# Optimization experiments

Measured on AMD Instinct MI355X. Metric: run time of the kernel, lower is better.

Reference implementation:

```python
import jax, jax.numpy as jnp
import numpy as np

B, T, N, D, H = 2, 12, 1024, 128, 8
HD = D // H  # head_dim = 16


def setup_inputs() -> dict:
    key = jax.random.key(0)
    ks = jax.random.split(key, 11)
    std = 0.02
    return {
        "query": jax.random.normal(ks[0], (B, T, N, D), dtype=jnp.float32),
        "key": jax.random.normal(ks[1], (B, T, N, D), dtype=jnp.float32),
        "value": jax.random.normal(ks[2], (B, T, N, D), dtype=jnp.float32),
        "Wq": jax.random.normal(ks[3], (D, D), dtype=jnp.float32) * std,
        "bq": jnp.zeros((D,), dtype=jnp.float32),
        "Wk": jax.random.normal(ks[4], (D, D), dtype=jnp.float32) * std,
        "bk": jnp.zeros((D,), dtype=jnp.float32),
        "Wv": jax.random.normal(ks[5], (D, D), dtype=jnp.float32) * std,
        "bv": jnp.zeros((D,), dtype=jnp.float32),
        "Wo": jax.random.normal(ks[6], (D, D), dtype=jnp.float32) * std,
        "bo": jnp.zeros((D,), dtype=jnp.float32),
    }


def reference(query, key, value, Wq, bq, Wk, bk, Wv, bv, Wo, bo):
    # Linear projections (torch nn.Linear: x @ W.T + b)
    q = query @ Wq.T + bq   # (B,T,N,D)
    k = key @ Wk.T + bk
    v = value @ Wv.T + bv
    # split heads: last dim D -> (H, HD)
    q = q.reshape(B, T, N, H, HD)
    k = k.reshape(B, T, N, H, HD)
    v = v.reshape(B, T, N, H, HD)
    scale = 1.0 / jnp.sqrt(jnp.float32(HD))
    # attention across node dim (N); scores (B,H,T,N,N) ~ 805 MB
    scores = jnp.einsum('btnhd,btmhd->bhtnm', q, k) * scale
    attn = jax.nn.softmax(scores, axis=-1)
    out = jnp.einsum('bhtnm,btmhd->btnhd', attn, v)  # (B,T,N,H,HD)
    out = out.reshape(B, T, N, D)
    return out @ Wo.T + bo
```

## Files before the change

### kernel.cpp

```cpp
#include <hip/hip_runtime.h>


#define DEV __device__ __forceinline__

typedef __attribute__((ext_vector_type(4))) float f32x4;
typedef __attribute__((ext_vector_type(8))) short s16x8;
typedef __attribute__((ext_vector_type(4))) short s16x4;
typedef __attribute__((ext_vector_type(2))) unsigned int u32x2;
typedef __attribute__((ext_vector_type(4))) unsigned int u32x4;

DEV unsigned short f2bf(float f) {
    unsigned u = __builtin_bit_cast(unsigned, f);
    u = (u + 0x7fffu + ((u >> 16) & 1u)) >> 16;
    return (unsigned short)u;
}

DEV unsigned pack_bf16(float a, float b) {
#if __has_builtin(__builtin_amdgcn_cvt_pk_bf16_f32)
    typedef __attribute__((ext_vector_type(2))) __bf16 bf16x2;
    bf16x2 t = __builtin_amdgcn_cvt_pk_bf16_f32(a, b);
    return __builtin_bit_cast(unsigned, t);
#else
    unsigned ua = __builtin_bit_cast(unsigned, a) + 0x8000u;
    unsigned ub = __builtin_bit_cast(unsigned, b) + 0x8000u;
    return __builtin_amdgcn_perm(ub, ua, 0x07060302);
#endif
}

DEV f32x4 mfma16(s16x4 a, s16x4 b, f32x4 c) {
#if __has_builtin(__builtin_amdgcn_mfma_f32_16x16x16bf16_1k)
    return __builtin_amdgcn_mfma_f32_16x16x16bf16_1k(a, b, c, 0, 0, 0);
#else
    s16x8 a8 = {a[0], a[1], a[2], a[3], 0, 0, 0, 0};
    s16x8 b8 = {b[0], b[1], b[2], b[3], 0, 0, 0, 0};
    return __builtin_amdgcn_mfma_f32_16x16x32_bf16(a8, b8, c, 0, 0, 0);
#endif
}

DEV f32x4 mfma32(s16x8 a, s16x8 b, f32x4 c) {
    return __builtin_amdgcn_mfma_f32_16x16x32_bf16(a, b, c, 0, 0, 0);
}

__global__ __launch_bounds__(256)
void wconv_kernel(const float* __restrict__ w0, const float* __restrict__ w1,
                  const float* __restrict__ w2, const float* __restrict__ w3,
                  unsigned short* __restrict__ o0, unsigned short* __restrict__ o1,
                  unsigned short* __restrict__ o2, unsigned short* __restrict__ o3)
{
    const int m = blockIdx.x >> 4;
    const float* W = (m == 0) ? w0 : (m == 1) ? w1 : (m == 2) ? w2 : w3;
    unsigned short* o = (m == 0) ? o0 : (m == 1) ? o1 : (m == 2) ? o2 : o3;
    const int idx = (blockIdx.x & 15) * 1024 + threadIdx.x * 4;
    float4 v = *(const float4*)(W + idx);
    ushort4 d;
    d.x = f2bf(v.x); d.y = f2bf(v.y); d.z = f2bf(v.z); d.w = f2bf(v.w);
    *(ushort4*)(o + idx) = d;
}

__global__ __launch_bounds__(256)
void qkv_proj_kernel(const float* __restrict__ xq, const float* __restrict__ xk,
                     const float* __restrict__ xv,
                     const unsigned short* __restrict__ Wqb,
                     const unsigned short* __restrict__ Wkb,
                     const unsigned short* __restrict__ Wvb,
                     const float* __restrict__ bq, const float* __restrict__ bk,
                     const float* __restrict__ bv,
                     unsigned short* __restrict__ oq, unsigned short* __restrict__ ok,
                     unsigned short* __restrict__ ov)
{
    const int z = blockIdx.y;
    const float* X    = (z == 0) ? xq : (z == 1) ? xk : xv;
    const unsigned short* Wb = (z == 0) ? Wqb : (z == 1) ? Wkb : Wvb;
    const float* bias = (z == 0) ? bq : (z == 1) ? bk : bv;
    unsigned short* out = (z == 0) ? oq : (z == 1) ? ok : ov;
    const float scale = (z == 0) ? 0.25f * 1.44269504088896f : 1.0f;

    __shared__ unsigned short Xs[64 * 136];
    __shared__ unsigned short Ws[128 * 136];

    const int t  = threadIdx.x;
    const int m0 = blockIdx.x * 64;

    {
        const float4* Xg = (const float4*)(X + (size_t)m0 * 128);
        #pragma unroll
        for (int p = 0; p < 8; p++) {
            int g = p * 256 + t;
            float4 vv = Xg[g];
            int row = g >> 5, c4 = g & 31;
            ushort4 d;
            d.x = f2bf(vv.x); d.y = f2bf(vv.y); d.z = f2bf(vv.z); d.w = f2bf(vv.w);
            *(ushort4*)&Xs[row * 136 + c4 * 4] = d;
        }
        #pragma unroll
        for (int p = 0; p < 8; p++) {
            int g = p * 256 + t, row = g >> 4, ch = g & 15;
            *(s16x8*)&Ws[row * 136 + ch * 8] =
                *(const s16x8*)(Wb + (size_t)row * 128 + ch * 8);
        }
    }
    __syncthreads();

    const int wave = t >> 6, lane = t & 63, quad = lane >> 4, n16 = lane & 15;
    f32x4 acc[8];
    const f32x4 zero4 = {0.f, 0.f, 0.f, 0.f};
    #pragma unroll
    for (int i = 0; i < 8; i++) acc[i] = zero4;

    #pragma unroll
    for (int ks = 0; ks < 4; ks++) {
        s16x8 a = *(const s16x8*)&Xs[(wave * 16 + n16) * 136 + ks * 32 + quad * 8];
        #pragma unroll
        for (int nt = 0; nt < 8; nt++) {
            s16x8 b = *(const s16x8*)&Ws[(nt * 16 + n16) * 136 + ks * 32 + quad * 8];
            acc[nt] = __builtin_amdgcn_mfma_f32_16x16x32_bf16(a, b, acc[nt], 0, 0, 0);
        }
    }

    const int bt    = m0 >> 10;
    const int nbase = (m0 & 1023) + wave * 16 + quad * 4;
    if (z == 2) {
        #pragma unroll
        for (int nt = 0; nt < 8; nt++) {
            float bb = bias[nt * 16 + n16];
            u32x2 pv = {pack_bf16(acc[nt][0] + bb, acc[nt][1] + bb),
                        pack_bf16(acc[nt][2] + bb, acc[nt][3] + bb)};
            *(u32x2*)&out[((size_t)(bt * 8 + nt) * 16 + n16) * 1024 + nbase] = pv;
        }
    } else {
        __syncthreads();
        const int crow = wave * 16 + quad * 4;
        #pragma unroll
        for (int nt = 0; nt < 8; nt++) {
            float bb = bias[nt * 16 + n16];
            #pragma unroll
            for (int r = 0; r < 4; r++)
                Xs[(crow + r) * 136 + nt * 16 + n16] = f2bf((acc[nt][r] + bb) * scale);
        }
        __syncthreads();
        #pragma unroll
        for (int p = 0; p < 4; p++) {
            int g = p * 256 + t, row = g >> 4, ch = g & 15;
            s16x8 val = *(const s16x8*)&Xs[row * 136 + ch * 8];
            *(s16x8*)&out[((size_t)(bt * 8 + (ch >> 1)) * 1024 + (m0 & 1023) + row) * 16
                          + (ch & 1) * 8] = val;
        }
    }
}

__global__ __launch_bounds__(256)
void attn_kernel(const unsigned short* __restrict__ q,
                 const unsigned short* __restrict__ k,
                 const unsigned short* __restrict__ vt,
                 unsigned short* __restrict__ O)
{
    __shared__ unsigned short Ks[2][256 * 20];
    __shared__ unsigned short VTs[2][16 * 264];

    const int t    = threadIdx.x;
    const int lane = t & 63, quad = lane >> 4, n16 = lane & 15;
    const int wave = t >> 6;
    const int bx = blockIdx.x, h = blockIdx.y, bt = blockIdx.z;
    const size_t headoff = (size_t)(bt * 8 + h) * 16384;
    const int q0 = bx * 64 + wave * 16;

    s16x4 qf = *(const s16x4*)(q + headoff + (size_t)(q0 + n16) * 16 + quad * 4);

    const f32x4 zero4 = {0.f, 0.f, 0.f, 0.f};
    f32x4 oacc = zero4, dacc = zero4;
    const s16x8 ones = {0x3F80, 0x3F80, 0x3F80, 0x3F80,
                        0x3F80, 0x3F80, 0x3F80, 0x3F80};
    const int krd0 = (8 * (n16 >> 2) + (n16 & 3)) * 20 + quad * 4;
    const int vrd  = n16 * 264 + quad * 8;
    const int krow = t >> 2, kseg = (t & 3) * 4;
    const int vrow = t >> 5, vseg = (t & 31) * 8;
    const unsigned short* kg = k  + headoff + (size_t)krow * 16 + kseg;
    const unsigned short* vg = vt + headoff + (size_t)vrow * 1024 + vseg;

    #pragma unroll
    for (int p = 0; p < 4; p++)
        *(s16x4*)&Ks[0][(p * 64 + krow) * 20 + kseg] =
            *(const s16x4*)(kg + (size_t)p * 1024);
    #pragma unroll
    for (int p = 0; p < 2; p++)
        *(s16x8*)&VTs[0][(p * 8 + vrow) * 264 + vseg] =
            *(const s16x8*)(vg + (size_t)p * 8192);

    #pragma unroll
    for (int c = 0; c < 4; c++) {
        __syncthreads();
        s16x4 kst[4];
        s16x8 vst[2];
        if (c < 3) {
            #pragma unroll
            for (int p = 0; p < 4; p++)
                kst[p] = *(const s16x4*)(kg + (size_t)((c + 1) * 256 + p * 64) * 16);
            #pragma unroll
            for (int p = 0; p < 2; p++)
                vst[p] = *(const s16x8*)(vg + (c + 1) * 256 + (size_t)p * 8192);
        }
        const unsigned short* Kc = Ks[c & 1];
        const unsigned short* Vc = VTs[c & 1];
        #pragma unroll
        for (int w = 0; w < 8; w++) {
            s16x4 kf0 = *(const s16x4*)&Kc[w * 640 + krd0];
            s16x4 kf1 = *(const s16x4*)&Kc[w * 640 + krd0 + 80];
            f32x4 s0 = mfma16(kf0, qf, zero4);
            f32x4 s1 = mfma16(kf1, qf, zero4);
            float p0 = __builtin_amdgcn_exp2f(s0[0]);
            float p1 = __builtin_amdgcn_exp2f(s0[1]);
            float p2 = __builtin_amdgcn_exp2f(s0[2]);
            float p3 = __builtin_amdgcn_exp2f(s0[3]);
            float p4 = __builtin_amdgcn_exp2f(s1[0]);
            float p5 = __builtin_amdgcn_exp2f(s1[1]);
            float p6 = __builtin_amdgcn_exp2f(s1[2]);
            float p7 = __builtin_amdgcn_exp2f(s1[3]);
            u32x4 pp = {pack_bf16(p0, p1), pack_bf16(p2, p3),
                        pack_bf16(p4, p5), pack_bf16(p6, p7)};
            s16x8 pf = __builtin_bit_cast(s16x8, pp);
            s16x8 vf = *(const s16x8*)&Vc[w * 32 + vrd];
            oacc = mfma32(pf, vf, oacc);
            dacc = mfma32(pf, ones, dacc);
        }
        if (c < 3) {
            unsigned short* Kn = Ks[(c + 1) & 1];
            unsigned short* Vn = VTs[(c + 1) & 1];
            #pragma unroll
            for (int p = 0; p < 4; p++)
                *(s16x4*)&Kn[(p * 64 + krow) * 20 + kseg] = kst[p];
            #pragma unroll
            for (int p = 0; p < 2; p++)
                *(s16x8*)&Vn[(p * 8 + vrow) * 264 + vseg] = vst[p];
        }
    }

    const int orow = q0 + quad * 4;
    #pragma unroll
    for (int r = 0; r < 4; r++) {
        float rv = oacc[r] * __builtin_amdgcn_rcpf(dacc[r]);
        O[((size_t)bt * 1024 + orow + r) * 128 + h * 16 + n16] = f2bf(rv);
    }
}

__global__ __launch_bounds__(256)
void o_proj_kernel(const unsigned short* __restrict__ X,
                   const unsigned short* __restrict__ Wb,
                   const float* __restrict__ bias, float* __restrict__ out)
{
    __shared__ unsigned short Xs[64 * 136];
    __shared__ unsigned short Ws[128 * 136];

    const int t  = threadIdx.x;
    const int m0 = blockIdx.x * 64;

    {
        #pragma unroll
        for (int p = 0; p < 4; p++) {
            int g = p * 256 + t, row = g >> 4, ch = g & 15;
            *(s16x8*)&Xs[row * 136 + ch * 8] =
                *(const s16x8*)(X + (size_t)(m0 + row) * 128 + ch * 8);
        }
        #pragma unroll
        for (int p = 0; p < 8; p++) {
            int g = p * 256 + t, row = g >> 4, ch = g & 15;
            *(s16x8*)&Ws[row * 136 + ch * 8] =
                *(const s16x8*)(Wb + (size_t)row * 128 + ch * 8);
        }
    }
    __syncthreads();

    const int wave = t >> 6, lane = t & 63, quad = lane >> 4, n16 = lane & 15;
    f32x4 acc[8];
    const f32x4 zero4 = {0.f, 0.f, 0.f, 0.f};
    #pragma unroll
    for (int i = 0; i < 8; i++) acc[i] = zero4;

    #pragma unroll
    for (int ks = 0; ks < 4; ks++) {
        s16x8 a = *(const s16x8*)&Xs[(wave * 16 + n16) * 136 + ks * 32 + quad * 8];
        #pragma unroll
        for (int nt = 0; nt < 8; nt++) {
            s16x8 b = *(const s16x8*)&Ws[(nt * 16 + n16) * 136 + ks * 32 + quad * 8];
            acc[nt] = __builtin_amdgcn_mfma_f32_16x16x32_bf16(a, b, acc[nt], 0, 0, 0);
        }
    }

    const int mrow = m0 + wave * 16 + quad * 4;
    #pragma unroll
    for (int nt = 0; nt < 8; nt++) {
        float bb = bias[nt * 16 + n16];
        #pragma unroll
        for (int r = 0; r < 4; r++)
            out[(size_t)(mrow + r) * 128 + nt * 16 + n16] = acc[nt][r] + bb;
    }
}

extern "C" void kernel_launch(void* const* d_in, const int* in_sizes, int n_in,
                              void* d_out, int out_size, void* d_ws, size_t ws_size,
                              hipStream_t stream)
{
    const float* query = (const float*)d_in[0];
    const float* key_  = (const float*)d_in[1];
    const float* value = (const float*)d_in[2];
    const float* Wq = (const float*)d_in[3];
    const float* bq = (const float*)d_in[4];
    const float* Wk = (const float*)d_in[5];
    const float* bk = (const float*)d_in[6];
    const float* Wv = (const float*)d_in[7];
    const float* bv = (const float*)d_in[8];
    const float* Wo = (const float*)d_in[9];
    const float* bo = (const float*)d_in[10];
    float* out = (float*)d_out;

    char* ws = (char*)d_ws;
    unsigned short* qb  = (unsigned short*)(ws);
    unsigned short* kb  = (unsigned short*)(ws + 6291456);
    unsigned short* vb  = (unsigned short*)(ws + 12582912);
    unsigned short* Ob  = (unsigned short*)(ws + 18874368);
    unsigned short* Wqb = (unsigned short*)(ws + 25165824);
    unsigned short* Wkb = (unsigned short*)(ws + 25198592);
    unsigned short* Wvb = (unsigned short*)(ws + 25231360);
    unsigned short* Wob = (unsigned short*)(ws + 25264128);

    wconv_kernel<<<dim3(64, 1, 1), 256, 0, stream>>>(
        Wq, Wk, Wv, Wo, Wqb, Wkb, Wvb, Wob);
    qkv_proj_kernel<<<dim3(384, 3, 1), 256, 0, stream>>>(
        query, key_, value, Wqb, Wkb, Wvb, bq, bk, bv, qb, kb, vb);
    attn_kernel<<<dim3(16, 8, 24), 256, 0, stream>>>(qb, kb, vb, Ob);
    o_proj_kernel<<<dim3(384, 1, 1), 256, 0, stream>>>(Ob, Wob, bo, out);
}
```

Baseline: 149.0 us.

## Load projection operands directly from global and shrink attention KV tiles

The QKV and output projection kernels no longer stage X and the weight matrix through shared memory. Each lane now loads its MFMA fragments straight from global memory, relying on cache for the weight reuse, which removes the LDS fill and a barrier. The attention kernel halves its K/V chunk from 256 to 128 keys and runs 8 pipelined iterations instead of 4, cutting shared-memory use so more blocks can be resident. The tradeoff is more global/L2 traffic with less coalesced loads in the projections, and more barriers per attention block.

```diff
diff --git a/kernel.cpp b/kernel.cpp
--- a/kernel.cpp
+++ b/kernel.cpp
@@ -75,44 +75,29 @@
     unsigned short* out = (z == 0) ? oq : (z == 1) ? ok : ov;
     const float scale = (z == 0) ? 0.25f * 1.44269504088896f : 1.0f;
 
-    __shared__ unsigned short Xs[64 * 136];
-    __shared__ unsigned short Ws[128 * 136];
+    __shared__ unsigned short Ts[64 * 136];
 
     const int t  = threadIdx.x;
     const int m0 = blockIdx.x * 64;
-
-    {
-        const float4* Xg = (const float4*)(X + (size_t)m0 * 128);
-        #pragma unroll
-        for (int p = 0; p < 8; p++) {
-            int g = p * 256 + t;
-            float4 vv = Xg[g];
-            int row = g >> 5, c4 = g & 31;
-            ushort4 d;
-            d.x = f2bf(vv.x); d.y = f2bf(vv.y); d.z = f2bf(vv.z); d.w = f2bf(vv.w);
-            *(ushort4*)&Xs[row * 136 + c4 * 4] = d;
-        }
-        #pragma unroll
-        for (int p = 0; p < 8; p++) {
-            int g = p * 256 + t, row = g >> 4, ch = g & 15;
-            *(s16x8*)&Ws[row * 136 + ch * 8] =
-                *(const s16x8*)(Wb + (size_t)row * 128 + ch * 8);
-        }
-    }
-    __syncthreads();
-
     const int wave = t >> 6, lane = t & 63, quad = lane >> 4, n16 = lane & 15;
+
     f32x4 acc[8];
     const f32x4 zero4 = {0.f, 0.f, 0.f, 0.f};
     #pragma unroll
     for (int i = 0; i < 8; i++) acc[i] = zero4;
 
+    const float* xrow = X + (size_t)(m0 + wave * 16 + n16) * 128 + quad * 8;
     #pragma unroll
     for (int ks = 0; ks < 4; ks++) {
-        s16x8 a = *(const s16x8*)&Xs[(wave * 16 + n16) * 136 + ks * 32 + quad * 8];
-        #pragma unroll
-        for (int nt = 0; nt < 8; nt++) {
-            s16x8 b = *(const s16x8*)&Ws[(nt * 16 + n16) * 136 + ks * 32 + quad * 8];
+        float4 xa = *(const float4*)(xrow + ks * 32);
+        float4 xb = *(const float4*)(xrow + ks * 32 + 4);
+        u32x4 av = {pack_bf16(xa.x, xa.y), pack_bf16(xa.z, xa.w),
+                    pack_bf16(xb.x, xb.y), pack_bf16(xb.z, xb.w)};
+        s16x8 a = __builtin_bit_cast(s16x8, av);
+        #pragma unroll
+        for (int nt = 0; nt < 8; nt++) {
+            s16x8 b = *(const s16x8*)(Wb + (size_t)(nt * 16 + n16) * 128
+                                         + ks * 32 + quad * 8);
             acc[nt] = __builtin_amdgcn_mfma_f32_16x16x32_bf16(a, b, acc[nt], 0, 0, 0);
         }
     }
@@ -128,20 +113,19 @@
             *(u32x2*)&out[((size_t)(bt * 8 + nt) * 16 + n16) * 1024 + nbase] = pv;
         }
     } else {
-        __syncthreads();
         const int crow = wave * 16 + quad * 4;
         #pragma unroll
         for (int nt = 0; nt < 8; nt++) {
             float bb = bias[nt * 16 + n16];
             #pragma unroll
             for (int r = 0; r < 4; r++)
-                Xs[(crow + r) * 136 + nt * 16 + n16] = f2bf((acc[nt][r] + bb) * scale);
+                Ts[(crow + r) * 136 + nt * 16 + n16] = f2bf((acc[nt][r] + bb) * scale);
         }
         __syncthreads();
         #pragma unroll
         for (int p = 0; p < 4; p++) {
             int g = p * 256 + t, row = g >> 4, ch = g & 15;
-            s16x8 val = *(const s16x8*)&Xs[row * 136 + ch * 8];
+            s16x8 val = *(const s16x8*)&Ts[row * 136 + ch * 8];
             *(s16x8*)&out[((size_t)(bt * 8 + (ch >> 1)) * 1024 + (m0 & 1023) + row) * 16
                           + (ch & 1) * 8] = val;
         }
@@ -154,8 +138,8 @@
                  const unsigned short* __restrict__ vt,
                  unsigned short* __restrict__ O)
 {
-    __shared__ unsigned short Ks[2][256 * 20];
-    __shared__ unsigned short VTs[2][16 * 264];
+    __shared__ unsigned short Ks[2][128 * 20];
+    __shared__ unsigned short VTs[2][16 * 136];
 
     const int t    = threadIdx.x;
     const int lane = t & 63, quad = lane >> 4, n16 = lane & 15;
@@ -171,38 +155,33 @@
     const s16x8 ones = {0x3F80, 0x3F80, 0x3F80, 0x3F80,
                         0x3F80, 0x3F80, 0x3F80, 0x3F80};
     const int krd0 = (8 * (n16 >> 2) + (n16 & 3)) * 20 + quad * 4;
-    const int vrd  = n16 * 264 + quad * 8;
+    const int vrd  = n16 * 136 + quad * 8;
     const int krow = t >> 2, kseg = (t & 3) * 4;
-    const int vrow = t >> 5, vseg = (t & 31) * 8;
+    const int vrow = t >> 4, vseg = (t & 15) * 8;
     const unsigned short* kg = k  + headoff + (size_t)krow * 16 + kseg;
     const unsigned short* vg = vt + headoff + (size_t)vrow * 1024 + vseg;
 
     #pragma unroll
-    for (int p = 0; p < 4; p++)
+    for (int p = 0; p < 2; p++)
         *(s16x4*)&Ks[0][(p * 64 + krow) * 20 + kseg] =
             *(const s16x4*)(kg + (size_t)p * 1024);
-    #pragma unroll
-    for (int p = 0; p < 2; p++)
-        *(s16x8*)&VTs[0][(p * 8 + vrow) * 264 + vseg] =
-            *(const s16x8*)(vg + (size_t)p * 8192);
-
-    #pragma unroll
-    for (int c = 0; c < 4; c++) {
+    *(s16x8*)&VTs[0][vrow * 136 + vseg] = *(const s16x8*)vg;
+
+    #pragma unroll
+    for (int c = 0; c < 8; c++) {
         __syncthreads();
-        s16x4 kst[4];
-        s16x8 vst[2];
-        if (c < 3) {
-            #pragma unroll
-            for (int p = 0; p < 4; p++)
-                kst[p] = *(const s16x4*)(kg + (size_t)((c + 1) * 256 + p * 64) * 16);
+        s16x4 kst[2];
+        s16x8 vst;
+        if (c < 7) {
             #pragma unroll
             for (int p = 0; p < 2; p++)
-                vst[p] = *(const s16x8*)(vg + (c + 1) * 256 + (size_t)p * 8192);
+                kst[p] = *(const s16x4*)(kg + (size_t)((c + 1) * 128 + p * 64) * 16);
+            vst = *(const s16x8*)(vg + (c + 1) * 128);
         }
         const unsigned short* Kc = Ks[c & 1];
         const unsigned short* Vc = VTs[c & 1];
         #pragma unroll
-        for (int w = 0; w < 8; w++) {
+        for (int w = 0; w < 4; w++) {
             s16x4 kf0 = *(const s16x4*)&Kc[w * 640 + krd0];
             s16x4 kf1 = *(const s16x4*)&Kc[w * 640 + krd0 + 80];
             f32x4 s0 = mfma16(kf0, qf, zero4);
@@ -222,15 +201,13 @@
             oacc = mfma32(pf, vf, oacc);
             dacc = mfma32(pf, ones, dacc);
         }
-        if (c < 3) {
+        if (c < 7) {
             unsigned short* Kn = Ks[(c + 1) & 1];
             unsigned short* Vn = VTs[(c + 1) & 1];
             #pragma unroll
-            for (int p = 0; p < 4; p++)
+            for (int p = 0; p < 2; p++)
                 *(s16x4*)&Kn[(p * 64 + krow) * 20 + kseg] = kst[p];
-            #pragma unroll
-            for (int p = 0; p < 2; p++)
-                *(s16x8*)&Vn[(p * 8 + vrow) * 264 + vseg] = vst[p];
+            *(s16x8*)&Vn[vrow * 136 + vseg] = vst;
         }
     }
 
@@ -247,40 +224,23 @@
                    const unsigned short* __restrict__ Wb,
                    const float* __restrict__ bias, float* __restrict__ out)
 {
-    __shared__ unsigned short Xs[64 * 136];
-    __shared__ unsigned short Ws[128 * 136];
-
     const int t  = threadIdx.x;
     const int m0 = blockIdx.x * 64;
-
-    {
-        #pragma unroll
-        for (int p = 0; p < 4; p++) {
-            int g = p * 256 + t, row = g >> 4, ch = g & 15;
-            *(s16x8*)&Xs[row * 136 + ch * 8] =
-                *(const s16x8*)(X + (size_t)(m0 + row) * 128 + ch * 8);
-        }
-        #pragma unroll
-        for (int p = 0; p < 8; p++) {
-            int g = p * 256 + t, row = g >> 4, ch = g & 15;
-            *(s16x8*)&Ws[row * 136 + ch * 8] =
-                *(const s16x8*)(Wb + (size_t)row * 128 + ch * 8);
-        }
-    }
-    __syncthreads();
-
     const int wave = t >> 6, lane = t & 63, quad = lane >> 4, n16 = lane & 15;
+
     f32x4 acc[8];
     const f32x4 zero4 = {0.f, 0.f, 0.f, 0.f};
     #pragma unroll
     for (int i = 0; i < 8; i++) acc[i] = zero4;
 
+    const unsigned short* xrow = X + (size_t)(m0 + wave * 16 + n16) * 128 + quad * 8;
     #pragma unroll
     for (int ks = 0; ks < 4; ks++) {
-        s16x8 a = *(const s16x8*)&Xs[(wave * 16 + n16) * 136 + ks * 32 + quad * 8];
-        #pragma unroll
-        for (int nt = 0; nt < 8; nt++) {
-            s16x8 b = *(const s16x8*)&Ws[(nt * 16 + n16) * 136 + ks * 32 + quad * 8];
+        s16x8 a = *(const s16x8*)(xrow + ks * 32);
+        #pragma unroll
+        for (int nt = 0; nt < 8; nt++) {
+            s16x8 b = *(const s16x8*)(Wb + (size_t)(nt * 16 + n16) * 128
+                                         + ks * 32 + quad * 8);
             acc[nt] = __builtin_amdgcn_mfma_f32_16x16x32_bf16(a, b, acc[nt], 0, 0, 0);
         }
     }
```

New measurement: 164.5 us. 10.4% more time.
